# Kernel optimization log

Measured on AMD Instinct MI355X. Metric: run time of the kernel, lower is better.

Reference implementation:

```python
import jax, jax.numpy as jnp
import numpy as np

DIM = 256
HEADS = 8
HEAD_DIM = 32
INNER = HEADS * HEAD_DIM  # 256
B, L_AG, H, W = 2, 5, 32, 32
SEQ = H * W
POS_HID = 32


def _lin(k, fan_in, fan_out):
    kw, kb = jax.random.split(k)
    Wt = jax.random.normal(kw, (fan_in, fan_out), jnp.float32) * (fan_in ** -0.5)
    b = jax.random.normal(kb, (fan_out,), jnp.float32) * 0.01
    return Wt, b


def setup_inputs() -> dict:
    key = jax.random.key(0)
    ks = jax.random.split(key, 10)
    x = jax.random.normal(ks[0], (B, L_AG, H, W, DIM), jnp.float32)
    Wq, bq = _lin(ks[1], DIM, INNER)
    Wk, bk = _lin(ks[2], DIM, INNER)
    Wv, bv = _lin(ks[3], DIM, INNER)
    Wp1, bp1 = _lin(ks[4], 3, POS_HID)
    Wp2, bp2 = _lin(ks[5], POS_HID, HEADS)
    Ws1, bs1 = _lin(ks[6], DIM, POS_HID)
    Ws2, bs2 = _lin(ks[7], POS_HID, HEADS)
    Wo, bo = _lin(ks[8], INNER, DIM)
    Wg, bg = _lin(ks[9], 2 * DIM, DIM)
    return dict(x=x, Wq=Wq, bq=bq, Wk=Wk, bk=bk, Wv=Wv, bv=bv,
                Wp1=Wp1, bp1=bp1, Wp2=Wp2, bp2=bp2,
                Ws1=Ws1, bs1=bs1, Ws2=Ws2, bs2=bs2,
                Wo=Wo, bo=bo, Wg=Wg, bg=bg)


def _relative_positions(h, w):
    # coords: (h*w, 2), row-major (i//w, i%w) like torch meshgrid 'ij'
    yy, xx = jnp.meshgrid(jnp.arange(h), jnp.arange(w), indexing='ij')
    coords = jnp.stack([yy.reshape(-1), xx.reshape(-1)], axis=-1)  # (L,2)
    rel = (coords[:, None, :] - coords[None, :, :]).astype(jnp.float32)  # (L,L,2)
    dist = jnp.linalg.norm(rel, axis=-1, keepdims=True)  # (L,L,1)
    return jnp.concatenate([rel, dist], axis=-1)  # (L,L,3)


def reference(x, Wq, bq, Wk, bk, Wv, bv, Wp1, bp1, Wp2, bp2,
              Ws1, bs1, Ws2, bs2, Wo, bo, Wg, bg):
    b, l, h, w, c = x.shape
    bl, L = b * l, h * w
    scale = HEAD_DIM ** -0.5
    x2 = x.reshape(bl, L, c)

    q = (x2 @ Wq + bq).reshape(bl, L, HEADS, HEAD_DIM)
    k = (x2 @ Wk + bk).reshape(bl, L, HEADS, HEAD_DIM)
    v = (x2 @ Wv + bv).reshape(bl, L, HEADS, HEAD_DIM)

    scores = jnp.einsum('bihd,bjhd->bhij', q, k) * scale  # (bl,H,L,L)

    rel_pos = _relative_positions(h, w)  # (L,L,3)
    pos_w = jax.nn.relu(rel_pos @ Wp1 + bp1) @ Wp2 + bp2  # (L,L,heads)
    pos_w = jnp.transpose(pos_w, (2, 0, 1))[None]  # (1,heads,L,L)

    s = jax.nn.relu(x2 @ Ws1 + bs1) @ Ws2 + bs2  # (bl,L,heads)
    fsim = jnp.einsum('bih,bjh->bij', s, s)[:, None]  # (bl,1,L,L)

    probs = jax.nn.softmax(scores + pos_w + fsim, axis=-1)
    out = jnp.einsum('bhij,bjhd->bihd', probs, v).reshape(bl, L, INNER)
    out = out @ Wo + bo  # (bl,L,dim); dropout is identity in eval

    gate = jax.nn.sigmoid(jnp.concatenate([x2, out], axis=-1) @ Wg + bg)
    out = gate * out + (1.0 - gate) * x2
    return out.reshape(b, l, h, w, c)
```

## Files before the change

### kernel.cpp

```cpp
#include <hip/hip_runtime.h>

typedef __bf16 bf16_t;
typedef __bf16 bf16x8 __attribute__((ext_vector_type(8)));
typedef float  f32x4  __attribute__((ext_vector_type(4)));

#define HEADS 8
#define HEAD_DIM 32
#define DIM 256
#define BL 10
#define SEQ 1024
#define M_TOTAL (BL*SEQ)
#define QK_SCALE 0.17677669529663687f
#define NPOS (63*63)

__device__ __forceinline__ int swz_idx(int row, int col) {
  return row*64 + (col ^ ((row & 7) << 3));
}
__device__ __forceinline__ int swz256(int row, int col) {
  return row*256 + (col ^ ((row & 7) << 3));
}

__global__ __launch_bounds__(256) void prep_kernel(
    const float* __restrict__ x,
    const float* __restrict__ Wq, const float* __restrict__ Wk, const float* __restrict__ Wv,
    const float* __restrict__ Wo, const float* __restrict__ Wg, const float* __restrict__ Ws1,
    const float* __restrict__ bq, const float* __restrict__ bk, const float* __restrict__ bv,
    const float* __restrict__ bs1,
    bf16_t* __restrict__ xb, bf16_t* __restrict__ btall,
    bf16_t* __restrict__ wot, bf16_t* __restrict__ wg1t, bf16_t* __restrict__ wg2t,
    float* __restrict__ bias_all)
{
  const int NX = M_TOTAL*DIM;
  const int NW = 65536;
  const int total = NX + 6*NW + 8192 + 8192 + 832;
  for (int i = blockIdx.x*blockDim.x + threadIdx.x; i < total; i += gridDim.x*blockDim.x) {
    int idx = i;
    if (idx < NX) { xb[idx] = (bf16_t)x[idx]; continue; }
    idx -= NX;
    if (idx < 6*NW) {
      const int a = idx >> 16, e = idx & 65535, n = e >> 8, k = e & 255;
      switch (a) {
        case 0: btall[n*256 + k]        = (bf16_t)Wq[k*256+n]; break;
        case 1: btall[(256+n)*256 + k]  = (bf16_t)Wk[k*256+n]; break;
        case 2: btall[(512+n)*256 + k]  = (bf16_t)Wv[k*256+n]; break;
        case 3: wot[n*256 + k]          = (bf16_t)Wo[k*256+n]; break;
        case 4: wg1t[n*256 + k]         = (bf16_t)Wg[k*256+n]; break;
        case 5: wg2t[n*256 + k]         = (bf16_t)Wg[(256+k)*256+n]; break;
      }
      continue;
    }
    idx -= 6*NW;
    if (idx < 8192) { const int m = idx >> 8, k = idx & 255;
      btall[(768+m)*256 + k] = (bf16_t)Ws1[k*32+m]; continue; }
    idx -= 8192;
    if (idx < 8192) { btall[(800*256) + idx] = (bf16_t)0.f; continue; }
    idx -= 8192;
    { const int j = idx;
      bias_all[j] = (j < 256) ? bq[j] : (j < 512) ? bk[j-256] :
                    (j < 768) ? bv[j-512] : (j < 800) ? bs1[j-768] : 0.f; }
  }
}

__global__ __launch_bounds__(256) void pos_tab_kernel(
    const float* __restrict__ Wp1, const float* __restrict__ bp1,
    const float* __restrict__ Wp2, const float* __restrict__ bp2,
    float* __restrict__ posT)
{
  __shared__ float w1[96], b1[32], w2[256], b2[8];
  const int tid = threadIdx.x;
  if (tid < 96) w1[tid] = Wp1[tid];
  if (tid < 32) b1[tid] = bp1[tid];
  w2[tid] = Wp2[tid];
  if (tid < 8)  b2[tid] = bp2[tid];
  __syncthreads();
  const int p = blockIdx.x*256 + tid;
  if (p >= NPOS) return;
  const float dy = (float)(p / 63 - 31);
  const float dx = (float)(p % 63 - 31);
  const float dist = sqrtf(dy*dy + dx*dx);
  float o[8];
  #pragma unroll
  for (int t = 0; t < 8; ++t) o[t] = b2[t];
  #pragma unroll
  for (int m = 0; m < 32; ++m) {
    float hv = fmaf(dy, w1[m], fmaf(dx, w1[32+m], fmaf(dist, w1[64+m], b1[m])));
    hv = fmaxf(hv, 0.f);
    #pragma unroll
    for (int t = 0; t < 8; ++t) o[t] = fmaf(hv, w2[m*8+t], o[t]);
  }
  #pragma unroll
  for (int t = 0; t < 8; ++t) posT[t*NPOS + p] = o[t];
}

__global__ __launch_bounds__(256) void qkv_kernel(
    const bf16_t* __restrict__ xb, const bf16_t* __restrict__ btall,
    const float* __restrict__ bias_all,
    bf16_t* __restrict__ qbuf, bf16_t* __restrict__ kbuf, bf16_t* __restrict__ vbuf,
    float* __restrict__ hidf)
{
  const int mt = blockIdx.x, ngb = blockIdx.y;
  const int tid = threadIdx.x;
  const int w = tid >> 6, lane = tid & 63, g = lane >> 4, l15 = lane & 15;
  const int arow = mt*64 + w*16 + l15;
  const bf16x8* Arow = (const bf16x8*)(xb + (size_t)arow*DIM);
  bf16x8 af[8];
  #pragma unroll
  for (int kc = 0; kc < 8; ++kc) af[kc] = Arow[kc*4 + g];
  const bool ishid = (ngb == 12);
  const int cmax = ishid ? 2 : 4;
  bf16_t* dst = (ngb < 4) ? qbuf : (ngb < 8) ? kbuf : vbuf;
  const int coloff = (ngb & 3) * 64;
  const float scale = (ngb < 4) ? QK_SCALE : 1.f;
  for (int c = 0; c < cmax; ++c) {
    const int n = ngb*64 + c*16 + l15;
    const bf16x8* Brow = (const bf16x8*)(btall + (size_t)n*DIM);
    f32x4 acc = {0.f,0.f,0.f,0.f};
    #pragma unroll
    for (int kc = 0; kc < 8; ++kc)
      acc = __builtin_amdgcn_mfma_f32_16x16x32_bf16(af[kc], Brow[kc*4+g], acc, 0, 0, 0);
    const float bvv = bias_all[n];
    #pragma unroll
    for (int r = 0; r < 4; ++r) {
      const int row = mt*64 + w*16 + g*4 + r;
      const float val = acc[r] + bvv;
      if (ishid) hidf[(size_t)row*32 + c*16 + l15] = fmaxf(val, 0.f);
      else dst[(size_t)row*DIM + coloff + c*16 + l15] = (bf16_t)(val*scale);
    }
  }
}

__global__ __launch_bounds__(256) void s2_kernel(
    const float* __restrict__ hidf, const float* __restrict__ Ws2,
    const float* __restrict__ bs2, float* __restrict__ sf)
{
  const int row = blockIdx.x*blockDim.x + threadIdx.x;
  if (row >= M_TOTAL) return;
  const float4* h4 = (const float4*)(hidf + (size_t)row*32);
  float sv[8];
  #pragma unroll
  for (int t = 0; t < 8; ++t) sv[t] = bs2[t];
  #pragma unroll
  for (int mq = 0; mq < 8; ++mq) {
    const float4 h = h4[mq];
    const float hv[4] = {h.x, h.y, h.z, h.w};
    #pragma unroll
    for (int e = 0; e < 4; ++e) {
      #pragma unroll
      for (int t = 0; t < 8; ++t) sv[t] = fmaf(hv[e], Ws2[(mq*4+e)*8+t], sv[t]);
    }
  }
  #pragma unroll
  for (int t = 0; t < 8; ++t) sf[(size_t)row*8+t] = sv[t];
}

__global__ __launch_bounds__(256) void attn_kernel(
    const bf16_t* __restrict__ qb, const bf16_t* __restrict__ kb,
    const bf16_t* __restrict__ vb, const float* __restrict__ sf,
    const float* __restrict__ posT, bf16_t* __restrict__ att)
{
  __shared__ __align__(16) bf16_t lqp[64*64];
  __shared__ __align__(16) bf16_t lk[64*64];
  __shared__ __align__(16) bf16_t lv[48*64];
  __shared__ float ptab[33*63];

  const int it = blockIdx.x, h = blockIdx.y, b = blockIdx.z;
  const int i0 = it*64, iy0 = it*2;
  const int tid = threadIdx.x;
  const int w = tid >> 6, lane = tid & 63, g = lane >> 4, l15 = lane & 15;

  for (int p = tid; p < 33*63; p += 256) {
    const int rr = p / 63, cc = p - rr*63;
    ptab[p] = posT[h*NPOS + (iy0 + rr)*63 + cc];
  }
  for (int p = tid; p < 16*64; p += 256) {
    const int d = 32 + (p >> 6), j = p & 63;
    lv[d*64 + (j ^ ((d & 7) << 3))] = (bf16_t)((d == 32) ? 1.f : 0.f);
  }
  {
    const int r = tid >> 2, q4 = tid & 3;
    const int grow = b*SEQ + i0 + r;
    #pragma unroll
    for (int cc = 0; cc < 2; ++cc) {
      const int ch = q4*2 + cc;
      bf16x8 v;
      if (ch < 4) {
        v = *(const bf16x8*)(qb + (size_t)grow*DIM + h*HEAD_DIM + ch*8);
      } else if (ch == 4) {
        const float* sp = sf + (size_t)grow*8;
        #pragma unroll
        for (int e = 0; e < 8; ++e) v[e] = (bf16_t)sp[e];
      } else {
        #pragma unroll
        for (int e = 0; e < 8; ++e) v[e] = (bf16_t)0.f;
      }
      *(bf16x8*)&lqp[swz_idx(r, ch*8)] = v;
    }
  }
  __syncthreads();

  const int qrow = w*16 + l15;
  const bf16x8 aq0 = *(const bf16x8*)&lqp[swz_idx(qrow, g*8)];
  const bf16x8 aq1 = *(const bf16x8*)&lqp[swz_idx(qrow, 32 + g*8)];

  f32x4 accO0 = {0.f,0.f,0.f,0.f}, accO1 = {0.f,0.f,0.f,0.f}, accO2 = {0.f,0.f,0.f,0.f};
  float mrow[4];
  #pragma unroll
  for (int r = 0; r < 4; ++r) mrow[r] = -1e30f;

  for (int jt = 0; jt < 16; ++jt) {
    const int j0 = jt*64;
    __syncthreads();
    {
      const int r = tid >> 2, q4 = tid & 3;
      const int grow = b*SEQ + j0 + r;
      #pragma unroll
      for (int cc = 0; cc < 2; ++cc) {
        const int ch = q4*2 + cc;
        bf16x8 v;
        if (ch < 4) {
          v = *(const bf16x8*)(kb + (size_t)grow*DIM + h*HEAD_DIM + ch*8);
        } else if (ch == 4) {
          const float* sp = sf + (size_t)grow*8;
          #pragma unroll
          for (int e = 0; e < 8; ++e) v[e] = (bf16_t)sp[e];
        } else {
          #pragma unroll
          for (int e = 0; e < 8; ++e) v[e] = (bf16_t)0.f;
        }
        *(bf16x8*)&lk[swz_idx(r, ch*8)] = v;
      }
    }
    {
      const int j = tid >> 2, q4 = tid & 3;
      const bf16x8 v = *(const bf16x8*)(vb + (size_t)(b*SEQ + j0 + j)*DIM + h*HEAD_DIM + q4*8);
      #pragma unroll
      for (int e = 0; e < 8; ++e) {
        const int d = q4*8 + e;
        lv[d*64 + (j ^ ((d & 7) << 3))] = v[e];
      }
    }
    __syncthreads();

    f32x4 s4[4];
    #pragma unroll
    for (int c = 0; c < 4; ++c) {
      const int krow = c*16 + l15;
      const bf16x8 bk0 = *(const bf16x8*)&lk[swz_idx(krow, g*8)];
      const bf16x8 bk1 = *(const bf16x8*)&lk[swz_idx(krow, 32 + g*8)];
      f32x4 acc = {0.f,0.f,0.f,0.f};
      acc = __builtin_amdgcn_mfma_f32_16x16x32_bf16(aq0, bk0, acc, 0, 0, 0);
      acc = __builtin_amdgcn_mfma_f32_16x16x32_bf16(aq1, bk1, acc, 0, 0, 0);
      s4[c] = acc;
    }

    const int ib = i0 + w*16 + g*4;
    #pragma unroll
    for (int r = 0; r < 4; ++r) {
      const int rbase = ((ib + r) >> 5) - iy0 + 31;
      const int ixr = (ib + r) & 31;
      #pragma unroll
      for (int c = 0; c < 4; ++c) {
        const int j = j0 + c*16 + l15;
        s4[c][r] += ptab[(rbase - (j >> 5))*63 + (ixr - (j & 31) + 31)];
      }
    }

    float pmax[4];
    #pragma unroll
    for (int r = 0; r < 4; ++r)
      pmax[r] = fmaxf(fmaxf(s4[0][r], s4[1][r]), fmaxf(s4[2][r], s4[3][r]));
    #pragma unroll
    for (int mk = 1; mk <= 8; mk <<= 1) {
      #pragma unroll
      for (int r = 0; r < 4; ++r)
        pmax[r] = fmaxf(pmax[r], __shfl_xor(pmax[r], mk));
    }
    float alpha[4];
    #pragma unroll
    for (int r = 0; r < 4; ++r) {
      const float mn = fmaxf(mrow[r], pmax[r]);
      alpha[r] = __expf(mrow[r] - mn);
      mrow[r] = mn;
    }
    #pragma unroll
    for (int r = 0; r < 4; ++r) {
      #pragma unroll
      for (int c = 0; c < 4; ++c) s4[c][r] = __expf(s4[c][r] - mrow[r]);
      accO0[r] *= alpha[r];
      accO1[r] *= alpha[r];
      accO2[r] *= alpha[r];
    }

    #pragma unroll
    for (int c = 0; c < 4; ++c) {
      #pragma unroll
      for (int r = 0; r < 4; ++r)
        lqp[swz_idx(w*16 + g*4 + r, c*16 + l15)] = (bf16_t)s4[c][r];
    }

    const int prow = w*16 + l15;
    #pragma unroll
    for (int kc = 0; kc < 2; ++kc) {
      const bf16x8 ap  = *(const bf16x8*)&lqp[swz_idx(prow, kc*32 + g*8)];
      const bf16x8 bv0 = *(const bf16x8*)&lv[swz_idx(l15,      kc*32 + g*8)];
      const bf16x8 bv1 = *(const bf16x8*)&lv[swz_idx(16 + l15, kc*32 + g*8)];
      const bf16x8 bv2 = *(const bf16x8*)&lv[swz_idx(32 + l15, kc*32 + g*8)];
      accO0 = __builtin_amdgcn_mfma_f32_16x16x32_bf16(ap, bv0, accO0, 0, 0, 0);
      accO1 = __builtin_amdgcn_mfma_f32_16x16x32_bf16(ap, bv1, accO1, 0, 0, 0);
      accO2 = __builtin_amdgcn_mfma_f32_16x16x32_bf16(ap, bv2, accO2, 0, 0, 0);
    }
  }

  #pragma unroll
  for (int r = 0; r < 4; ++r) {
    const int row = b*SEQ + i0 + w*16 + g*4 + r;
    const float lsum = __shfl(accO2[r], lane & 48);
    const float inv = 1.f / lsum;
    att[(size_t)row*DIM + h*HEAD_DIM + l15]      = (bf16_t)(accO0[r]*inv);
    att[(size_t)row*DIM + h*HEAD_DIM + 16 + l15] = (bf16_t)(accO1[r]*inv);
  }
}

__global__ __launch_bounds__(256) void prjgate_kernel(
    const bf16_t* __restrict__ att, const bf16_t* __restrict__ wot,
    const float* __restrict__ bo, const bf16_t* __restrict__ xb,
    const float* __restrict__ x, const bf16_t* __restrict__ wg1t,
    const bf16_t* __restrict__ wg2t, const float* __restrict__ bg,
    float* __restrict__ outp)
{
  __shared__ __align__(16) bf16_t prjT[16*256];
  const int row0 = blockIdx.x * 16;
  const int tid = threadIdx.x;
  const int w = tid >> 6, lane = tid & 63, g = lane >> 4, l15 = lane & 15;
  const int arow = row0 + l15;

  {
    const bf16x8* Arow = (const bf16x8*)(att + (size_t)arow*DIM);
    bf16x8 afA[8];
    #pragma unroll
    for (int kc = 0; kc < 8; ++kc) afA[kc] = Arow[kc*4 + g];
    #pragma unroll
    for (int ct = 0; ct < 4; ++ct) {
      const int n = w*64 + ct*16 + l15;
      const bf16x8* Brow = (const bf16x8*)(wot + (size_t)n*DIM);
      f32x4 acc = {0.f,0.f,0.f,0.f};
      #pragma unroll
      for (int kc = 0; kc < 8; ++kc)
        acc = __builtin_amdgcn_mfma_f32_16x16x32_bf16(afA[kc], Brow[kc*4+g], acc, 0, 0, 0);
      const float bvo = bo[n];
      #pragma unroll
      for (int r = 0; r < 4; ++r)
        prjT[swz256(g*4 + r, n)] = (bf16_t)(acc[r] + bvo);
    }
  }
  __syncthreads();

  const bf16x8* A1r = (const bf16x8*)(xb + (size_t)arow*DIM);
  bf16x8 a1[8], a2[8];
  #pragma unroll
  for (int kc = 0; kc < 8; ++kc) {
    a1[kc] = A1r[kc*4 + g];
    a2[kc] = *(const bf16x8*)&prjT[swz256(l15, kc*32 + g*8)];
  }
  #pragma unroll
  for (int ct = 0; ct < 4; ++ct) {
    const int n = w*64 + ct*16 + l15;
    const bf16x8* b1 = (const bf16x8*)(wg1t + (size_t)n*DIM);
    const bf16x8* b2 = (const bf16x8*)(wg2t + (size_t)n*DIM);
    f32x4 acc = {0.f,0.f,0.f,0.f};
    #pragma unroll
    for (int kc = 0; kc < 8; ++kc)
      acc = __builtin_amdgcn_mfma_f32_16x16x32_bf16(a1[kc], b1[kc*4+g], acc, 0, 0, 0);
    #pragma unroll
    for (int kc = 0; kc < 8; ++kc)
      acc = __builtin_amdgcn_mfma_f32_16x16x32_bf16(a2[kc], b2[kc*4+g], acc, 0, 0, 0);
    const float bgv = bg[n];
    #pragma unroll
    for (int r = 0; r < 4; ++r) {
      const int grow = row0 + g*4 + r;
      const float gate = 1.f / (1.f + __expf(-(acc[r] + bgv)));
      const float pv = (float)prjT[swz256(g*4 + r, n)];
      const float xv = x[(size_t)grow*DIM + n];
      outp[(size_t)grow*DIM + n] = gate*pv + (1.f - gate)*xv;
    }
  }
}

extern "C" void kernel_launch(void* const* d_in, const int* in_sizes, int n_in,
                              void* d_out, int out_size, void* d_ws, size_t ws_size,
                              hipStream_t stream)
{
  const float* x   = (const float*)d_in[0];
  const float* Wq  = (const float*)d_in[1];
  const float* bq  = (const float*)d_in[2];
  const float* Wk  = (const float*)d_in[3];
  const float* bk  = (const float*)d_in[4];
  const float* Wv  = (const float*)d_in[5];
  const float* bv  = (const float*)d_in[6];
  const float* Wp1 = (const float*)d_in[7];
  const float* bp1 = (const float*)d_in[8];
  const float* Wp2 = (const float*)d_in[9];
  const float* bp2 = (const float*)d_in[10];
  const float* Ws1 = (const float*)d_in[11];
  const float* bs1 = (const float*)d_in[12];
  const float* Ws2 = (const float*)d_in[13];
  const float* bs2 = (const float*)d_in[14];
  const float* Wo  = (const float*)d_in[15];
  const float* bo  = (const float*)d_in[16];
  const float* Wg  = (const float*)d_in[17];
  const float* bg  = (const float*)d_in[18];

  char* ws = (char*)d_ws;
  size_t off = 0;
  auto alloc = [&](size_t bytes) {
    char* p = ws + off;
    off += (bytes + 255) & ~(size_t)255;
    return p;
  };
  bf16_t* xb    = (bf16_t*)alloc((size_t)M_TOTAL*DIM*2);
  bf16_t* qbuf  = (bf16_t*)alloc((size_t)M_TOTAL*DIM*2);
  bf16_t* kbuf  = (bf16_t*)alloc((size_t)M_TOTAL*DIM*2);
  bf16_t* vbuf  = (bf16_t*)alloc((size_t)M_TOTAL*DIM*2);
  bf16_t* att   = (bf16_t*)alloc((size_t)M_TOTAL*DIM*2);
  bf16_t* btall = (bf16_t*)alloc((size_t)832*256*2);
  bf16_t* wot   = (bf16_t*)alloc(65536*2);
  bf16_t* wg1t  = (bf16_t*)alloc(65536*2);
  bf16_t* wg2t  = (bf16_t*)alloc(65536*2);
  float*  bias_all = (float*)alloc(832*4);
  float*  hidf  = (float*)alloc((size_t)M_TOTAL*32*4);
  float*  sfb   = (float*)alloc((size_t)M_TOTAL*8*4);
  float*  posT  = (float*)alloc((size_t)HEADS*NPOS*4);
  (void)ws_size; (void)in_sizes; (void)n_in; (void)out_size;

  prep_kernel<<<2048, 256, 0, stream>>>(x, Wq, Wk, Wv, Wo, Wg, Ws1, bq, bk, bv, bs1,
                                        xb, btall, wot, wg1t, wg2t, bias_all);
  pos_tab_kernel<<<(NPOS+255)/256, 256, 0, stream>>>(Wp1, bp1, Wp2, bp2, posT);
  qkv_kernel<<<dim3(M_TOTAL/64, 13), 256, 0, stream>>>(xb, btall, bias_all,
                                                       qbuf, kbuf, vbuf, hidf);
  s2_kernel<<<M_TOTAL/256, 256, 0, stream>>>(hidf, Ws2, bs2, sfb);
  attn_kernel<<<dim3(SEQ/64, HEADS, BL), 256, 0, stream>>>(qbuf, kbuf, vbuf, sfb, posT, att);
  prjgate_kernel<<<M_TOTAL/16, 256, 0, stream>>>(att, wot, bo, xb, x, wg1t, wg2t, bg,
                                                 (float*)d_out);
}
```

Before: 179.0 us.

## Split weight prep into vectorized cast and tiled transpose, prefetch K/V in attention

The single grid-stride prep kernel is replaced by two kernels. One does a float4-vectorized cast of x plus the Ws1 and bias packing. The other does a shared-memory tiled transpose of the six 256x256 weight matrices, giving coalesced reads and writes. The attention kernel now prefetches the next K/V/s tile into registers while computing on the current one. It also hoists the constant zero padding of the K tile out of the loop and remaps the flattened block index so each XCD handles a contiguous (batch, head) range for better L2 locality. The zero-filled padding rows 800–831 of btall are no longer allocated or written, so qkv_kernel may read whatever lies past row 800 if it still touches them.

```diff
diff --git a/kernel.cpp b/kernel.cpp
--- a/kernel.cpp
+++ b/kernel.cpp
@@ -1,6 +1,7 @@
 #include <hip/hip_runtime.h>
 
 typedef __bf16 bf16_t;
+typedef __bf16 bf16x4 __attribute__((ext_vector_type(4)));
 typedef __bf16 bf16x8 __attribute__((ext_vector_type(8)));
 typedef float  f32x4  __attribute__((ext_vector_type(4)));
 
@@ -20,44 +21,64 @@
   return row*256 + (col ^ ((row & 7) << 3));
 }
 
-__global__ __launch_bounds__(256) void prep_kernel(
-    const float* __restrict__ x,
+__global__ __launch_bounds__(256) void cast_kernel(
+    const float* __restrict__ x, const float* __restrict__ Ws1,
+    const float* __restrict__ bq, const float* __restrict__ bk,
+    const float* __restrict__ bv, const float* __restrict__ bs1,
+    bf16_t* __restrict__ xb, bf16_t* __restrict__ btall, float* __restrict__ bias_all)
+{
+  const int NX4 = M_TOTAL*DIM/4;
+  const int i = blockIdx.x*blockDim.x + threadIdx.x;
+  if (i < NX4) {
+    const float4 v = ((const float4*)x)[i];
+    bf16x4 o; o[0]=(bf16_t)v.x; o[1]=(bf16_t)v.y; o[2]=(bf16_t)v.z; o[3]=(bf16_t)v.w;
+    *(bf16x4*)(xb + (size_t)i*4) = o;
+    return;
+  }
+  int idx = i - NX4;
+  if (idx < 8192) {
+    const int m = idx >> 8, k = idx & 255;
+    btall[(768 + m)*256 + k] = (bf16_t)Ws1[k*32 + m];
+    return;
+  }
+  idx -= 8192;
+  if (idx < 832) {
+    bias_all[idx] = (idx < 256) ? bq[idx] : (idx < 512) ? bk[idx-256] :
+                    (idx < 768) ? bv[idx-512] : (idx < 800) ? bs1[idx-768] : 0.f;
+  }
+}
+
+__global__ __launch_bounds__(256) void trans_kernel(
     const float* __restrict__ Wq, const float* __restrict__ Wk, const float* __restrict__ Wv,
-    const float* __restrict__ Wo, const float* __restrict__ Wg, const float* __restrict__ Ws1,
-    const float* __restrict__ bq, const float* __restrict__ bk, const float* __restrict__ bv,
-    const float* __restrict__ bs1,
-    bf16_t* __restrict__ xb, bf16_t* __restrict__ btall,
-    bf16_t* __restrict__ wot, bf16_t* __restrict__ wg1t, bf16_t* __restrict__ wg2t,
-    float* __restrict__ bias_all)
-{
-  const int NX = M_TOTAL*DIM;
-  const int NW = 65536;
-  const int total = NX + 6*NW + 8192 + 8192 + 832;
-  for (int i = blockIdx.x*blockDim.x + threadIdx.x; i < total; i += gridDim.x*blockDim.x) {
-    int idx = i;
-    if (idx < NX) { xb[idx] = (bf16_t)x[idx]; continue; }
-    idx -= NX;
-    if (idx < 6*NW) {
-      const int a = idx >> 16, e = idx & 65535, n = e >> 8, k = e & 255;
-      switch (a) {
-        case 0: btall[n*256 + k]        = (bf16_t)Wq[k*256+n]; break;
-        case 1: btall[(256+n)*256 + k]  = (bf16_t)Wk[k*256+n]; break;
-        case 2: btall[(512+n)*256 + k]  = (bf16_t)Wv[k*256+n]; break;
-        case 3: wot[n*256 + k]          = (bf16_t)Wo[k*256+n]; break;
-        case 4: wg1t[n*256 + k]         = (bf16_t)Wg[k*256+n]; break;
-        case 5: wg2t[n*256 + k]         = (bf16_t)Wg[(256+k)*256+n]; break;
-      }
-      continue;
-    }
-    idx -= 6*NW;
-    if (idx < 8192) { const int m = idx >> 8, k = idx & 255;
-      btall[(768+m)*256 + k] = (bf16_t)Ws1[k*32+m]; continue; }
-    idx -= 8192;
-    if (idx < 8192) { btall[(800*256) + idx] = (bf16_t)0.f; continue; }
-    idx -= 8192;
-    { const int j = idx;
-      bias_all[j] = (j < 256) ? bq[j] : (j < 512) ? bk[j-256] :
-                    (j < 768) ? bv[j-512] : (j < 800) ? bs1[j-768] : 0.f; }
+    const float* __restrict__ Wo, const float* __restrict__ Wg,
+    bf16_t* __restrict__ btall, bf16_t* __restrict__ wot,
+    bf16_t* __restrict__ wg1t, bf16_t* __restrict__ wg2t)
+{
+  __shared__ float tile[64][65];
+  const float* src; bf16_t* dst;
+  switch (blockIdx.z) {
+    case 0: src = Wq;         dst = btall;          break;
+    case 1: src = Wk;         dst = btall + 65536;  break;
+    case 2: src = Wv;         dst = btall + 131072; break;
+    case 3: src = Wo;         dst = wot;            break;
+    case 4: src = Wg;         dst = wg1t;           break;
+    default: src = Wg + 65536; dst = wg2t;          break;
+  }
+  const int bi = blockIdx.x, bj = blockIdx.y;
+  const int t = threadIdx.x, tr = t >> 4, tc = t & 15;
+  #pragma unroll
+  for (int i = 0; i < 4; ++i) {
+    const float4 v = *(const float4*)(src + (size_t)(bi*64 + tr + 16*i)*256 + bj*64 + tc*4);
+    float* tp = &tile[tr + 16*i][tc*4];
+    tp[0]=v.x; tp[1]=v.y; tp[2]=v.z; tp[3]=v.w;
+  }
+  __syncthreads();
+  #pragma unroll
+  for (int i = 0; i < 4; ++i) {
+    bf16x4 o;
+    #pragma unroll
+    for (int e = 0; e < 4; ++e) o[e] = (bf16_t)tile[tc*4 + e][tr + 16*i];
+    *(bf16x4*)(dst + (size_t)(bj*64 + tr + 16*i)*256 + bi*64 + tc*4) = o;
   }
 }
 
@@ -163,10 +184,23 @@
   __shared__ __align__(16) bf16_t lv[48*64];
   __shared__ float ptab[33*63];
 
-  const int it = blockIdx.x, h = blockIdx.y, b = blockIdx.z;
+  const int wg = blockIdx.x;
+  const int xcd = wg & 7, within = wg >> 3;
+  const int pair = xcd*10 + (within >> 4);
+  const int it = within & 15;
+  const int h = pair & 7, b = pair >> 3;
   const int i0 = it*64, iy0 = it*2;
   const int tid = threadIdx.x;
   const int w = tid >> 6, lane = tid & 63, g = lane >> 4, l15 = lane & 15;
+  const int r4 = tid >> 2, q4 = tid & 3;
+
+  bf16x8 kreg = *(const bf16x8*)(kb + (size_t)(b*SEQ + r4)*DIM + h*HEAD_DIM + q4*8);
+  bf16x8 vreg = *(const bf16x8*)(vb + (size_t)(b*SEQ + r4)*DIM + h*HEAD_DIM + q4*8);
+  float4 sA, sB;
+  if (tid < 64) {
+    const float* sp = sf + (size_t)(b*SEQ + tid)*8;
+    sA = *(const float4*)sp; sB = *(const float4*)(sp + 4);
+  }
 
   for (int p = tid; p < 33*63; p += 256) {
     const int rr = p / 63, cc = p - rr*63;
@@ -176,9 +210,15 @@
     const int d = 32 + (p >> 6), j = p & 63;
     lv[d*64 + (j ^ ((d & 7) << 3))] = (bf16_t)((d == 32) ? 1.f : 0.f);
   }
+  for (int p = tid; p < 192; p += 256) {
+    const int rr = p / 3, ch = 5 + (p % 3);
+    bf16x8 z;
+    #pragma unroll
+    for (int e = 0; e < 8; ++e) z[e] = (bf16_t)0.f;
+    *(bf16x8*)&lk[swz_idx(rr, ch*8)] = z;
+  }
   {
-    const int r = tid >> 2, q4 = tid & 3;
-    const int grow = b*SEQ + i0 + r;
+    const int grow = b*SEQ + i0 + r4;
     #pragma unroll
     for (int cc = 0; cc < 2; ++cc) {
       const int ch = q4*2 + cc;
@@ -193,7 +233,7 @@
         #pragma unroll
         for (int e = 0; e < 8; ++e) v[e] = (bf16_t)0.f;
       }
-      *(bf16x8*)&lqp[swz_idx(r, ch*8)] = v;
+      *(bf16x8*)&lqp[swz_idx(r4, ch*8)] = v;
     }
   }
   __syncthreads();
@@ -210,36 +250,29 @@
   for (int jt = 0; jt < 16; ++jt) {
     const int j0 = jt*64;
     __syncthreads();
-    {
-      const int r = tid >> 2, q4 = tid & 3;
-      const int grow = b*SEQ + j0 + r;
-      #pragma unroll
-      for (int cc = 0; cc < 2; ++cc) {
-        const int ch = q4*2 + cc;
-        bf16x8 v;
-        if (ch < 4) {
-          v = *(const bf16x8*)(kb + (size_t)grow*DIM + h*HEAD_DIM + ch*8);
-        } else if (ch == 4) {
-          const float* sp = sf + (size_t)grow*8;
-          #pragma unroll
-          for (int e = 0; e < 8; ++e) v[e] = (bf16_t)sp[e];
-        } else {
-          #pragma unroll
-          for (int e = 0; e < 8; ++e) v[e] = (bf16_t)0.f;
-        }
-        *(bf16x8*)&lk[swz_idx(r, ch*8)] = v;
+    *(bf16x8*)&lk[swz_idx(r4, q4*8)] = kreg;
+    #pragma unroll
+    for (int e = 0; e < 8; ++e) {
+      const int d = q4*8 + e;
+      lv[d*64 + (r4 ^ ((d & 7) << 3))] = vreg[e];
+    }
+    if (tid < 64) {
+      bf16x8 sv;
+      sv[0]=(bf16_t)sA.x; sv[1]=(bf16_t)sA.y; sv[2]=(bf16_t)sA.z; sv[3]=(bf16_t)sA.w;
+      sv[4]=(bf16_t)sB.x; sv[5]=(bf16_t)sB.y; sv[6]=(bf16_t)sB.z; sv[7]=(bf16_t)sB.w;
+      *(bf16x8*)&lk[swz_idx(tid, 32)] = sv;
+    }
+    __syncthreads();
+
+    if (jt < 15) {
+      const int grow = b*SEQ + j0 + 64 + r4;
+      kreg = *(const bf16x8*)(kb + (size_t)grow*DIM + h*HEAD_DIM + q4*8);
+      vreg = *(const bf16x8*)(vb + (size_t)grow*DIM + h*HEAD_DIM + q4*8);
+      if (tid < 64) {
+        const float* sp = sf + (size_t)(b*SEQ + j0 + 64 + tid)*8;
+        sA = *(const float4*)sp; sB = *(const float4*)(sp + 4);
       }
     }
-    {
-      const int j = tid >> 2, q4 = tid & 3;
-      const bf16x8 v = *(const bf16x8*)(vb + (size_t)(b*SEQ + j0 + j)*DIM + h*HEAD_DIM + q4*8);
-      #pragma unroll
-      for (int e = 0; e < 8; ++e) {
-        const int d = q4*8 + e;
-        lv[d*64 + (j ^ ((d & 7) << 3))] = v[e];
-      }
-    }
-    __syncthreads();
 
     f32x4 s4[4];
     #pragma unroll
@@ -422,7 +455,7 @@
   bf16_t* kbuf  = (bf16_t*)alloc((size_t)M_TOTAL*DIM*2);
   bf16_t* vbuf  = (bf16_t*)alloc((size_t)M_TOTAL*DIM*2);
   bf16_t* att   = (bf16_t*)alloc((size_t)M_TOTAL*DIM*2);
-  bf16_t* btall = (bf16_t*)alloc((size_t)832*256*2);
+  bf16_t* btall = (bf16_t*)alloc((size_t)800*256*2);
   bf16_t* wot   = (bf16_t*)alloc(65536*2);
   bf16_t* wg1t  = (bf16_t*)alloc(65536*2);
   bf16_t* wg2t  = (bf16_t*)alloc(65536*2);
@@ -432,13 +465,16 @@
   float*  posT  = (float*)alloc((size_t)HEADS*NPOS*4);
   (void)ws_size; (void)in_sizes; (void)n_in; (void)out_size;
 
-  prep_kernel<<<2048, 256, 0, stream>>>(x, Wq, Wk, Wv, Wo, Wg, Ws1, bq, bk, bv, bs1,
-                                        xb, btall, wot, wg1t, wg2t, bias_all);
+  const int cast_total = M_TOTAL*DIM/4 + 8192 + 832;
+  cast_kernel<<<(cast_total + 255)/256, 256, 0, stream>>>(x, Ws1, bq, bk, bv, bs1,
+                                                          xb, btall, bias_all);
+  trans_kernel<<<dim3(4,4,6), 256, 0, stream>>>(Wq, Wk, Wv, Wo, Wg,
+                                                btall, wot, wg1t, wg2t);
   pos_tab_kernel<<<(NPOS+255)/256, 256, 0, stream>>>(Wp1, bp1, Wp2, bp2, posT);
   qkv_kernel<<<dim3(M_TOTAL/64, 13), 256, 0, stream>>>(xb, btall, bias_all,
                                                        qbuf, kbuf, vbuf, hidf);
   s2_kernel<<<M_TOTAL/256, 256, 0, stream>>>(hidf, Ws2, bs2, sfb);
-  attn_kernel<<<dim3(SEQ/64, HEADS, BL), 256, 0, stream>>>(qbuf, kbuf, vbuf, sfb, posT, att);
+  attn_kernel<<<SEQ/64*HEADS*BL, 256, 0, stream>>>(qbuf, kbuf, vbuf, sfb, posT, att);
   prjgate_kernel<<<M_TOTAL/16, 256, 0, stream>>>(att, wot, bo, xb, x, wg1t, wg2t, bg,
                                                  (float*)d_out);
 }
```

Measured after the change: 167.2 us. -6.6%, faster.
